# Performance work log

Hardware: AMD Instinct MI355X
Metric: run time of the kernel (lower is better)

The kernel has to match this reference:

```python
import jax, jax.numpy as jnp
import numpy as np
from functools import reduce

N_QUBITS = 12
DIM = 2 ** N_QUBITS          # 4096 state-vector dimension
DEPTH = 6                    # ansatz rotation layers
BATCH = 256
OBSERVE_BITS = (0, 1, 2)     # Pauli-Z expectation on these qubits
INPUT_SCALING = np.pi


def setup_inputs() -> dict:
    key = jax.random.key(0)
    k1, k2 = jax.random.split(key)
    input_tensor = jax.random.uniform(k1, (BATCH, N_QUBITS), dtype=jnp.float32)
    # param_init_range = (-pi/depth, pi/depth)
    thetas = jax.random.normal(k2, (DEPTH, N_QUBITS), dtype=jnp.float32) * (np.pi / DEPTH)
    return {"input_tensor": input_tensor, "thetas": thetas}


def _ry(theta):
    # RY(theta) = [[cos t/2, -sin t/2], [sin t/2, cos t/2]]
    h = theta * 0.5
    c, s = jnp.cos(h), jnp.sin(h)
    return jnp.stack([jnp.stack([c, -s]), jnp.stack([s, c])]).astype(jnp.complex64)


def _cnot_ladder_perm():
    # CNOT(i -> i+1) for i = 0..n-2; each CNOT is a basis permutation that
    # flips the target bit when the control bit is 1. Compose permutations
    # (applied in reverse order so state_out = state_in[perm]). Qubit 0 is the
    # leftmost kron factor, i.e. bit position n-1-q of the basis index.
    perm = np.arange(DIM)
    for cq, tq in reversed([(i, i + 1) for i in range(N_QUBITS - 1)]):
        cbit, tbit = N_QUBITS - 1 - cq, N_QUBITS - 1 - tq
        flip = ((perm >> cbit) & 1) == 1
        perm = np.where(flip, perm ^ (1 << tbit), perm)
    return jnp.asarray(perm)


_PERM = _cnot_ladder_perm()


def _forward(input_tensor, thetas):
    # --- encoder: RY(pi * x_q) applied to |0...0> gives a product state ---
    half = input_tensor * (INPUT_SCALING * 0.5)          # [B, n] half-angles
    c, s = jnp.cos(half), jnp.sin(half)
    psi = jnp.ones((BATCH, 1), dtype=jnp.complex64)
    for q in range(N_QUBITS):                            # fixed small loop over qubits
        amp = jnp.stack([c[:, q], s[:, q]], axis=-1).astype(jnp.complex64)  # [B, 2]
        psi = (psi[:, :, None] * amp[:, None, :]).reshape(BATCH, -1)
    state = psi.T                                        # [DIM, B] complex64

    # --- ansatz: per-depth full-unitary (kron of per-qubit gates) mm, then CNOT ladder ---
    for d in range(DEPTH):
        U = reduce(jnp.kron, [_ry(thetas[d, q]) for q in range(N_QUBITS)])  # [DIM, DIM]
        state = U @ state                                # Hamiltonian @ state (torch.mm)
        state = state[_PERM]                             # entangling CNOT ladder

    # --- observer: <Z_q> on each observed qubit ---
    probs = state.real ** 2 + state.imag ** 2            # [DIM, B]
    idx = jnp.arange(DIM)
    zdiag = jnp.stack([1.0 - 2.0 * ((idx >> (N_QUBITS - 1 - q)) & 1)
                       for q in OBSERVE_BITS]).astype(jnp.float32)          # [K, DIM]
    return jnp.einsum('kn,nb->bk', zdiag, probs)         # [B, K]


def reference(input_tensor, thetas):
    return _forward(input_tensor, thetas)
```

## Files before the change

### kernel.cpp

```cpp
#include <hip/hip_runtime.h>
#include <math.h>
#include <type_traits>

#define NQ     12
#define DIM    4096
#define DEPTH  6
#define NBATCH 256
#define NT     512
#define NREG   8


__host__ __device__ constexpr unsigned axmask(int d, int b) {
    unsigned m = 1u << b;
    for (int i = 0; i < d; ++i) m = (m ^ (m >> 1)) & 0xFFFu;
    return m;
}
__host__ __device__ constexpr unsigned selmask(int d, int b) {
    unsigned m = 1u << b;
    for (int i = 0; i < 16 - d; ++i) m = (m ^ ((m << 1) & 0xFFFu)) & 0xFFFu;
    return m;
}
__host__ __device__ constexpr int cpopc(unsigned v) {
    int c = 0; while (v) { c += (int)(v & 1u); v >>= 1; } return c;
}

template<int I, int N, class F>
__device__ __forceinline__ void sfor(F&& f) {
    if constexpr (I < N) {
        f(std::integral_constant<int, I>{});
        sfor<I + 1, N>(static_cast<F&&>(f));
    }
}

template<int CTRL>
__device__ __forceinline__ float dppx(float v) {
    int iv = __float_as_int(v);
    return __int_as_float(__builtin_amdgcn_update_dpp(iv, iv, CTRL, 0xF, 0xF, false));
}
template<int M4>
__device__ __forceinline__ float lxor_low(float v) {
    static_assert(M4 >= 1 && M4 <= 15, "low mask");
    if constexpr      (M4 == 1)  return dppx<0xB1>(v);
    else if constexpr (M4 == 2)  return dppx<0x4E>(v);
    else if constexpr (M4 == 3)  return dppx<0x1B>(v);
    else if constexpr (M4 == 7)  return dppx<0x141>(v);
    else if constexpr (M4 == 15) return dppx<0x140>(v);
    else if constexpr ((M4 & 8) == 0)
        return lxor_low<M4 ^ 7>(dppx<0x141>(v));
    else
        return lxor_low<M4 ^ 15>(dppx<0x140>(v));
}
template<int MASK>
__device__ __forceinline__ float lxor(float v) {
    static_assert(MASK > 0 && MASK < 64, "lane mask");
    if constexpr (MASK >= 32) {
        return __shfl_xor(v, MASK, 64);
    } else if constexpr (MASK >= 16) {
        return __int_as_float(__builtin_amdgcn_ds_swizzle(__float_as_int(v),
                                                          (MASK << 10) | 0x1F));
    } else {
        return lxor_low<MASK>(v);
    }
}

__device__ __forceinline__ int lad(int t, int k) {
    return t * 8 + 4 * (k ^ ((t >> 2) & 1));
}

template<int D, int B>
__device__ __forceinline__ void gate_reg(float (&st)[NREG], int tid, float t) {
    constexpr unsigned V = axmask(D, B), M = selmask(D, B);
    static_assert((V >> 3) == 0 && V != 0, "reg gate");
    constexpr int VR = (int)V;
    constexpr unsigned MR = M & 7u, MT = M >> 3;
    const float tp = (__popc(MT & (unsigned)tid) & 1) ? t : -t;
    const float tn = -tp;
    sfor<0, NREG>([&](auto RC) {
        constexpr int r = RC.value, r2 = r ^ VR;
        if constexpr (r2 > r) {
            constexpr bool p0 = (cpopc(MR & (unsigned)r)  & 1) != 0;
            constexpr bool p1 = (cpopc(MR & (unsigned)r2) & 1) != 0;
            float a0 = st[r];
            st[r]  = fmaf(p0 ? tn : tp, st[r2], st[r]);
            st[r2] = fmaf(p1 ? tn : tp, a0,     st[r2]);
        }
    });
}

template<int D, int B>
__device__ __forceinline__ void gate_lane(float (&st)[NREG], int tid, float t) {
    constexpr unsigned V = axmask(D, B), M = selmask(D, B);
    constexpr int VT = (int)(V >> 3), VR = (int)(V & 7u);
    static_assert(VT > 0 && VT < 64, "intra-wave gate");
    static_assert((M & 7u) == 0, "no reg bits in selector for b>=3");
    const float tp = (__popc((M >> 3) & (unsigned)tid) & 1) ? t : -t;
    if constexpr (VR == 0) {
        sfor<0, NREG>([&](auto RC) {
            constexpr int r = RC.value;
            float p = lxor<VT>(st[r]);
            st[r] = fmaf(tp, p, st[r]);
        });
    } else {
        sfor<0, NREG>([&](auto RC) {
            constexpr int r = RC.value, r2 = r ^ VR;
            if constexpr (r2 > r) {
                float pa = lxor<VT>(st[r2]);
                float pb = lxor<VT>(st[r]);
                st[r]  = fmaf(tp, pa, st[r]);
                st[r2] = fmaf(tp, pb, st[r2]);
            }
        });
    }
}

template<int D>
__device__ __forceinline__ void gate9x(float (&st)[NREG], int tid, float t,
                                       float* __restrict__ lds9) {
    constexpr unsigned V = axmask(D, 9), M = selmask(D, 9);
    static_assert((V & 7u) == 0 && (M & 7u) == 0, "b9 reg-pure-free");
    constexpr int T = (int)(V >> 3);
    static_assert(T >= 64 && T < 512, "b9 crosses waves");
    const float tp = (__popc((M >> 3) & (unsigned)tid) & 1) ? t : -t;
    float* buf = lds9 + (D & 1) * DIM;
    sfor<0, 2>([&](auto KC) {
        constexpr int k = KC.value;
        *reinterpret_cast<float4*>(&buf[lad(tid, k)]) =
            make_float4(st[4*k], st[4*k+1], st[4*k+2], st[4*k+3]);
    });
    __syncthreads();
    const int p = tid ^ T;
    sfor<0, 2>([&](auto KC) {
        constexpr int k = KC.value;
        float4 pv = *reinterpret_cast<const float4*>(&buf[lad(p, k)]);
        st[4*k+0] = fmaf(tp, pv.x, st[4*k+0]);
        st[4*k+1] = fmaf(tp, pv.y, st[4*k+1]);
        st[4*k+2] = fmaf(tp, pv.z, st[4*k+2]);
        st[4*k+3] = fmaf(tp, pv.w, st[4*k+3]);
    });
}

template<int D>
__device__ __forceinline__ void cross2(float (&st)[NREG], int tid,
                                       float t1, float t2,
                                       float* __restrict__ lds2) {
    constexpr unsigned V1 = axmask(D, 11), V2 = axmask(D, 10);
    constexpr unsigned M1 = selmask(D, 11), M2 = selmask(D, 10);
    static_assert((V1 & 7u) == 0 && (V2 & 7u) == 0, "cross axes reg-free");
    static_assert((M1 & 7u) == 0 && (M2 & 7u) == 0, "cross masks reg-free");
    constexpr int T1 = (int)(V1 >> 3), T2 = (int)(V2 >> 3);
    static_assert((cpopc(M1 & V2) & 1) == 0, "kC sign identity");

    const float t1p = (__popc((M1 >> 3) & (unsigned)tid) & 1) ? t1 : -t1;
    const float t2p = (__popc((M2 >> 3) & (unsigned)tid) & 1) ? t2 : -t2;
    const float t12 = t1p * t2p;

    float* buf = lds2 + (D & 1) * DIM;
    sfor<0, 2>([&](auto KC) {
        constexpr int k = KC.value;
        *reinterpret_cast<float4*>(&buf[lad(tid, k)]) =
            make_float4(st[4*k], st[4*k+1], st[4*k+2], st[4*k+3]);
    });
    __syncthreads();
    const int p1 = tid ^ T1, p2 = tid ^ T2, p3 = tid ^ (T1 ^ T2);
    sfor<0, 2>([&](auto KC) {
        constexpr int k = KC.value;
        float4 A  = *reinterpret_cast<const float4*>(&buf[lad(p1, k)]);
        float4 Bv = *reinterpret_cast<const float4*>(&buf[lad(p2, k)]);
        float4 Cv = *reinterpret_cast<const float4*>(&buf[lad(p3, k)]);
        float t;
        t = fmaf(t1p, A.x, st[4*k+0]); t = fmaf(t2p, Bv.x, t); st[4*k+0] = fmaf(t12, Cv.x, t);
        t = fmaf(t1p, A.y, st[4*k+1]); t = fmaf(t2p, Bv.y, t); st[4*k+1] = fmaf(t12, Cv.y, t);
        t = fmaf(t1p, A.z, st[4*k+2]); t = fmaf(t2p, Bv.z, t); st[4*k+2] = fmaf(t12, Cv.z, t);
        t = fmaf(t1p, A.w, st[4*k+3]); t = fmaf(t2p, Bv.w, t); st[4*k+3] = fmaf(t12, Cv.w, t);
    });
}

template<int D>
__device__ __forceinline__ void depth_apply(float (&st)[NREG], int tid,
                                            const float* __restrict__ tsh,
                                            float* __restrict__ lds2,
                                            float* __restrict__ lds9) {
    float4 ta = *reinterpret_cast<const float4*>(&tsh[D * 12 + 0]);
    float4 tb = *reinterpret_cast<const float4*>(&tsh[D * 12 + 4]);
    float4 tc = *reinterpret_cast<const float4*>(&tsh[D * 12 + 8]);
    float tq[12] = {ta.x, ta.y, ta.z, ta.w, tb.x, tb.y, tb.z, tb.w,
                    tc.x, tc.y, tc.z, tc.w};
    cross2<D>(st, tid, tq[0], tq[1], lds2);
    gate9x<D>(st, tid, tq[2], lds9);
    sfor<3, 12>([&](auto QC) {
        constexpr int Q = QC.value, B = 11 - Q;
        if constexpr (B >= 3) gate_lane<D, B>(st, tid, tq[Q]);
        else                  gate_reg <D, B>(st, tid, tq[Q]);
    });
}

__global__ __launch_bounds__(NT, 2)
void qnet_kernel(const float* __restrict__ x,
                 const float* __restrict__ thetas,
                 float* __restrict__ out)
{
    __shared__ __align__(16) float lds2[2 * DIM];
    __shared__ __align__(16) float lds9[2 * DIM];
    __shared__ __align__(16) float tsh[80];
    __shared__ __align__(16) float csh[80];
    __shared__ float red[8];

    const int b   = blockIdx.x;
    const int tid = threadIdx.x;

    if (tid < 72) {
        float rev = thetas[tid] * 0.07957747154594767f;
        float cc  = __builtin_amdgcn_cosf(rev);
        float ss  = __builtin_amdgcn_sinf(rev);
        csh[tid] = cc;
        tsh[tid] = ss * __builtin_amdgcn_rcpf(cc);
    }

    const float4* xv = reinterpret_cast<const float4*>(x + b * 12);
    float4 xa = xv[0], xb = xv[1], xc = xv[2];
    float xs[12] = {xa.x, xa.y, xa.z, xa.w, xb.x, xb.y, xb.z, xb.w,
                    xc.x, xc.y, xc.z, xc.w};
    float cq[12], sq[12];
    sfor<0, 12>([&](auto QC) {
        constexpr int q = QC.value;
        float rev = xs[q] * 0.25f;
        sq[q] = __builtin_amdgcn_sinf(rev);
        cq[q] = __builtin_amdgcn_cosf(rev);
    });

    float la = 1.0f;
    sfor<0, 9>([&](auto IC) {
        constexpr int i = IC.value;
        la *= ((tid >> i) & 1) ? sq[8 - i] : cq[8 - i];
    });
    float st[NREG];
    st[0] = la;
    sfor<0, 3>([&](auto IC) {
        constexpr int i = IC.value;
        sfor<0, (1 << i)>([&](auto KC) {
            constexpr int k = KC.value;
            float base = st[k];
            st[k + (1 << i)] = base * sq[11 - i];
            st[k]            = base * cq[11 - i];
        });
    });

    __syncthreads();

    sfor<0, 6>([&](auto DC) {
        depth_apply<DC.value>(st, tid, tsh, lds2, lds9);
    });

    float sc = 1.0f;
    sfor<0, 18>([&](auto IC) {
        constexpr int i = IC.value;
        float4 c4 = *reinterpret_cast<const float4*>(&csh[4 * i]);
        sc *= (c4.x * c4.y) * (c4.z * c4.w);
    });

    float tot = 0.0f;
    sfor<0, NREG>([&](auto RC) {
        constexpr int r = RC.value;
        tot = fmaf(st[r], st[r], tot);
    });
    tot *= sc * sc;

    float v = tot;
    v += lxor<1>(v);
    v += lxor<2>(v);
    v += lxor<4>(v);
    v += lxor<8>(v);
    v += lxor<16>(v);
    v += lxor<32>(v);
    const int w = tid >> 6;
    if ((tid & 63) == 0) red[w] = v;
    __syncthreads();
    if (tid < 3) {
        float acc = 0.0f;
        #pragma unroll
        for (int ww = 0; ww < 8; ++ww) {
            int par = (tid == 0) ? ((ww >> 2) & 1)
                    : (tid == 1) ? ((ww >> 1) & 1)
                    :              (((ww >> 2) ^ ww) & 1);
            acc += par ? -red[ww] : red[ww];
        }
        out[b * 3 + tid] = acc;
    }
}

extern "C" void kernel_launch(void* const* d_in, const int* in_sizes, int n_in,
                              void* d_out, int out_size, void* d_ws, size_t ws_size,
                              hipStream_t stream) {
    (void)in_sizes; (void)n_in; (void)out_size; (void)d_ws; (void)ws_size;
    const float* x      = (const float*)d_in[0];
    const float* thetas = (const float*)d_in[1];
    float* out          = (float*)d_out;

    qnet_kernel<<<dim3(NBATCH), dim3(NT), 0, stream>>>(x, thetas, out);
}
```

Before: 14.41 us.

## Fuse three cross-thread qubit gates into one LDS exchange and use permlane swaps

Merges the separate qubit-9 LDS exchange into the existing two-qubit cross-wave step, so each depth applies the three cross-thread gates as a single 8-term combination after one shared-memory store and one barrier. This removes one __syncthreads and one store/read round per depth and halves LDS allocation, which may help occupancy. In exchange each thread now reads seven float4 neighbours instead of three plus one, raising LDS read traffic and FMA count. It also replaces shfl_xor/ds_swizzle lane exchanges with permlane16/32 swap builtins when the compiler provides them, and decomposes masks that span several lane bits.

```diff
diff --git a/kernel.cpp b/kernel.cpp
--- a/kernel.cpp
+++ b/kernel.cpp
@@ -8,6 +8,16 @@
 #define NBATCH 256
 #define NT     512
 #define NREG   8
+
+#if defined(__has_builtin)
+#  if __has_builtin(__builtin_amdgcn_permlane16_swap) && __has_builtin(__builtin_amdgcn_permlane32_swap)
+#    define USE_PERMLANE 1
+#  else
+#    define USE_PERMLANE 0
+#  endif
+#else
+#  define USE_PERMLANE 0
+#endif
 
 
 __host__ __device__ constexpr unsigned axmask(int d, int b) {
@@ -50,6 +60,29 @@
     else
         return lxor_low<M4 ^ 15>(dppx<0x140>(v));
 }
+
+#if USE_PERMLANE
+typedef unsigned u32x2 __attribute__((ext_vector_type(2)));
+__device__ __forceinline__ float plx16(float v) {
+    unsigned u = __float_as_uint(v);
+    u32x2 r = __builtin_amdgcn_permlane16_swap(u, u, false, false);
+    return __uint_as_float(r[0] ^ r[1] ^ u);
+}
+__device__ __forceinline__ float plx32(float v) {
+    unsigned u = __float_as_uint(v);
+    u32x2 r = __builtin_amdgcn_permlane32_swap(u, u, false, false);
+    return __uint_as_float(r[0] ^ r[1] ^ u);
+}
+template<int MASK>
+__device__ __forceinline__ float lxor(float v) {
+    static_assert(MASK > 0 && MASK < 64, "lane mask");
+    float r = v;
+    if constexpr (MASK & 32) r = plx32(r);
+    if constexpr (MASK & 16) r = plx16(r);
+    if constexpr (MASK & 15) r = lxor_low<MASK & 15>(r);
+    return r;
+}
+#else
 template<int MASK>
 __device__ __forceinline__ float lxor(float v) {
     static_assert(MASK > 0 && MASK < 64, "lane mask");
@@ -62,6 +95,7 @@
         return lxor_low<MASK>(v);
     }
 }
+#endif
 
 __device__ __forceinline__ int lad(int t, int k) {
     return t * 8 + 4 * (k ^ ((t >> 2) & 1));
@@ -114,45 +148,27 @@
 }
 
 template<int D>
-__device__ __forceinline__ void gate9x(float (&st)[NREG], int tid, float t,
-                                       float* __restrict__ lds9) {
-    constexpr unsigned V = axmask(D, 9), M = selmask(D, 9);
-    static_assert((V & 7u) == 0 && (M & 7u) == 0, "b9 reg-pure-free");
-    constexpr int T = (int)(V >> 3);
-    static_assert(T >= 64 && T < 512, "b9 crosses waves");
-    const float tp = (__popc((M >> 3) & (unsigned)tid) & 1) ? t : -t;
-    float* buf = lds9 + (D & 1) * DIM;
-    sfor<0, 2>([&](auto KC) {
-        constexpr int k = KC.value;
-        *reinterpret_cast<float4*>(&buf[lad(tid, k)]) =
-            make_float4(st[4*k], st[4*k+1], st[4*k+2], st[4*k+3]);
-    });
-    __syncthreads();
-    const int p = tid ^ T;
-    sfor<0, 2>([&](auto KC) {
-        constexpr int k = KC.value;
-        float4 pv = *reinterpret_cast<const float4*>(&buf[lad(p, k)]);
-        st[4*k+0] = fmaf(tp, pv.x, st[4*k+0]);
-        st[4*k+1] = fmaf(tp, pv.y, st[4*k+1]);
-        st[4*k+2] = fmaf(tp, pv.z, st[4*k+2]);
-        st[4*k+3] = fmaf(tp, pv.w, st[4*k+3]);
-    });
-}
-
-template<int D>
-__device__ __forceinline__ void cross2(float (&st)[NREG], int tid,
-                                       float t1, float t2,
+__device__ __forceinline__ void cross3(float (&st)[NREG], int tid,
+                                       float t1, float t2, float t9,
                                        float* __restrict__ lds2) {
-    constexpr unsigned V1 = axmask(D, 11), V2 = axmask(D, 10);
-    constexpr unsigned M1 = selmask(D, 11), M2 = selmask(D, 10);
-    static_assert((V1 & 7u) == 0 && (V2 & 7u) == 0, "cross axes reg-free");
-    static_assert((M1 & 7u) == 0 && (M2 & 7u) == 0, "cross masks reg-free");
-    constexpr int T1 = (int)(V1 >> 3), T2 = (int)(V2 >> 3);
-    static_assert((cpopc(M1 & V2) & 1) == 0, "kC sign identity");
-
-    const float t1p = (__popc((M1 >> 3) & (unsigned)tid) & 1) ? t1 : -t1;
-    const float t2p = (__popc((M2 >> 3) & (unsigned)tid) & 1) ? t2 : -t2;
-    const float t12 = t1p * t2p;
+    constexpr unsigned V1 = axmask(D, 11), V2 = axmask(D, 10), V9 = axmask(D, 9);
+    constexpr unsigned M1 = selmask(D, 11), M2 = selmask(D, 10), M9 = selmask(D, 9);
+    static_assert(((V1 | V2 | V9) & 7u) == 0, "cross axes reg-free");
+    static_assert(((M1 | M2 | M9) & 7u) == 0, "cross masks reg-free");
+    constexpr int T1 = (int)(V1 >> 3), T2 = (int)(V2 >> 3), T9 = (int)(V9 >> 3);
+    static_assert(T1 > 0 && T2 > 0 && T9 > 0, "thread-crossing");
+    constexpr int p12 = cpopc(M2 & V1) & 1;
+    constexpr int p19 = cpopc(M9 & V1) & 1;
+    constexpr int p29 = cpopc(M9 & V2) & 1;
+    constexpr int p123 = (p12 + cpopc(M9 & (V1 ^ V2))) & 1;
+
+    const float e1 = (__popc((M1 >> 3) & (unsigned)tid) & 1) ? t1 : -t1;
+    const float e2 = (__popc((M2 >> 3) & (unsigned)tid) & 1) ? t2 : -t2;
+    const float e9 = (__popc((M9 >> 3) & (unsigned)tid) & 1) ? t9 : -t9;
+    const float k12  = (p12  ? -1.f : 1.f) * e1 * e2;
+    const float k19  = (p19  ? -1.f : 1.f) * e1 * e9;
+    const float k29  = (p29  ? -1.f : 1.f) * e2 * e9;
+    const float k123 = (p123 ? -1.f : 1.f) * e1 * e2 * e9;
 
     float* buf = lds2 + (D & 1) * DIM;
     sfor<0, 2>([&](auto KC) {
@@ -161,32 +177,49 @@
             make_float4(st[4*k], st[4*k+1], st[4*k+2], st[4*k+3]);
     });
     __syncthreads();
-    const int p1 = tid ^ T1, p2 = tid ^ T2, p3 = tid ^ (T1 ^ T2);
+    const int q1 = tid ^ T1,        q2 = tid ^ T2,        q9 = tid ^ T9;
+    const int q12 = tid ^ (T1^T2),  q19 = tid ^ (T1^T9),  q29 = tid ^ (T2^T9);
+    const int q123 = tid ^ (T1^T2^T9);
     sfor<0, 2>([&](auto KC) {
         constexpr int k = KC.value;
-        float4 A  = *reinterpret_cast<const float4*>(&buf[lad(p1, k)]);
-        float4 Bv = *reinterpret_cast<const float4*>(&buf[lad(p2, k)]);
-        float4 Cv = *reinterpret_cast<const float4*>(&buf[lad(p3, k)]);
-        float t;
-        t = fmaf(t1p, A.x, st[4*k+0]); t = fmaf(t2p, Bv.x, t); st[4*k+0] = fmaf(t12, Cv.x, t);
-        t = fmaf(t1p, A.y, st[4*k+1]); t = fmaf(t2p, Bv.y, t); st[4*k+1] = fmaf(t12, Cv.y, t);
-        t = fmaf(t1p, A.z, st[4*k+2]); t = fmaf(t2p, Bv.z, t); st[4*k+2] = fmaf(t12, Cv.z, t);
-        t = fmaf(t1p, A.w, st[4*k+3]); t = fmaf(t2p, Bv.w, t); st[4*k+3] = fmaf(t12, Cv.w, t);
+        float4 A1 = *reinterpret_cast<const float4*>(&buf[lad(q1,   k)]);
+        float4 A2 = *reinterpret_cast<const float4*>(&buf[lad(q2,   k)]);
+        float4 A9 = *reinterpret_cast<const float4*>(&buf[lad(q9,   k)]);
+        float4 B2 = *reinterpret_cast<const float4*>(&buf[lad(q12,  k)]);
+        float4 B9 = *reinterpret_cast<const float4*>(&buf[lad(q19,  k)]);
+        float4 C9 = *reinterpret_cast<const float4*>(&buf[lad(q29,  k)]);
+        float4 Dv = *reinterpret_cast<const float4*>(&buf[lad(q123, k)]);
+        sfor<0, 4>([&](auto EC) {
+            constexpr int e = EC.value;
+            const float a1 = (e==0)?A1.x:(e==1)?A1.y:(e==2)?A1.z:A1.w;
+            const float a2 = (e==0)?A2.x:(e==1)?A2.y:(e==2)?A2.z:A2.w;
+            const float a9 = (e==0)?A9.x:(e==1)?A9.y:(e==2)?A9.z:A9.w;
+            const float b2 = (e==0)?B2.x:(e==1)?B2.y:(e==2)?B2.z:B2.w;
+            const float b9 = (e==0)?B9.x:(e==1)?B9.y:(e==2)?B9.z:B9.w;
+            const float c9 = (e==0)?C9.x:(e==1)?C9.y:(e==2)?C9.z:C9.w;
+            const float dv = (e==0)?Dv.x:(e==1)?Dv.y:(e==2)?Dv.z:Dv.w;
+            float t = st[4*k+e];
+            t = fmaf(e1,   a1, t);
+            t = fmaf(e2,   a2, t);
+            t = fmaf(e9,   a9, t);
+            t = fmaf(k12,  b2, t);
+            t = fmaf(k19,  b9, t);
+            t = fmaf(k29,  c9, t);
+            st[4*k+e] = fmaf(k123, dv, t);
+        });
     });
 }
 
 template<int D>
 __device__ __forceinline__ void depth_apply(float (&st)[NREG], int tid,
                                             const float* __restrict__ tsh,
-                                            float* __restrict__ lds2,
-                                            float* __restrict__ lds9) {
+                                            float* __restrict__ lds2) {
     float4 ta = *reinterpret_cast<const float4*>(&tsh[D * 12 + 0]);
     float4 tb = *reinterpret_cast<const float4*>(&tsh[D * 12 + 4]);
     float4 tc = *reinterpret_cast<const float4*>(&tsh[D * 12 + 8]);
     float tq[12] = {ta.x, ta.y, ta.z, ta.w, tb.x, tb.y, tb.z, tb.w,
                     tc.x, tc.y, tc.z, tc.w};
-    cross2<D>(st, tid, tq[0], tq[1], lds2);
-    gate9x<D>(st, tid, tq[2], lds9);
+    cross3<D>(st, tid, tq[0], tq[1], tq[2], lds2);
     sfor<3, 12>([&](auto QC) {
         constexpr int Q = QC.value, B = 11 - Q;
         if constexpr (B >= 3) gate_lane<D, B>(st, tid, tq[Q]);
@@ -200,7 +233,6 @@
                  float* __restrict__ out)
 {
     __shared__ __align__(16) float lds2[2 * DIM];
-    __shared__ __align__(16) float lds9[2 * DIM];
     __shared__ __align__(16) float tsh[80];
     __shared__ __align__(16) float csh[80];
     __shared__ float red[8];
@@ -248,7 +280,7 @@
     __syncthreads();
 
     sfor<0, 6>([&](auto DC) {
-        depth_apply<DC.value>(st, tid, tsh, lds2, lds9);
+        depth_apply<DC.value>(st, tid, tsh, lds2);
     });
 
     float sc = 1.0f;
```

New measurement: 16.42 us. 14.0% more time.

## Use 1024 threads with 4 amplitudes each and pair high-qubit gates via LDS

Applied to the files above, without the earlier changes.

Doubles the threads per block to 1024 and halves the per-thread register state from 8 to 4 amplitudes, remapping the qubit-to-thread/register bit layout. The single-qubit cross-wave gate for bit 9 is folded with bit 8 into a second fused two-gate LDS exchange, so each depth still uses two LDS barriers. The aim is more parallelism and shorter per-thread serial gate chains. The cost is larger reductions (16 waves), one block per CU, and more shuffle traffic per amplitude.

```diff
diff --git a/kernel.cpp b/kernel.cpp
--- a/kernel.cpp
+++ b/kernel.cpp
@@ -6,8 +6,8 @@
 #define DIM    4096
 #define DEPTH  6
 #define NBATCH 256
-#define NT     512
-#define NREG   8
+#define NT     1024
+#define NREG   4
 
 
 __host__ __device__ constexpr unsigned axmask(int d, int b) {
@@ -63,16 +63,12 @@
     }
 }
 
-__device__ __forceinline__ int lad(int t, int k) {
-    return t * 8 + 4 * (k ^ ((t >> 2) & 1));
-}
-
 template<int D, int B>
 __device__ __forceinline__ void gate_reg(float (&st)[NREG], int tid, float t) {
     constexpr unsigned V = axmask(D, B), M = selmask(D, B);
-    static_assert((V >> 3) == 0 && V != 0, "reg gate");
+    static_assert((V >> 2) == 0 && V != 0, "reg gate");
     constexpr int VR = (int)V;
-    constexpr unsigned MR = M & 7u, MT = M >> 3;
+    constexpr unsigned MR = M & 3u, MT = M >> 2;
     const float tp = (__popc(MT & (unsigned)tid) & 1) ? t : -t;
     const float tn = -tp;
     sfor<0, NREG>([&](auto RC) {
@@ -90,10 +86,10 @@
 template<int D, int B>
 __device__ __forceinline__ void gate_lane(float (&st)[NREG], int tid, float t) {
     constexpr unsigned V = axmask(D, B), M = selmask(D, B);
-    constexpr int VT = (int)(V >> 3), VR = (int)(V & 7u);
+    constexpr int VT = (int)(V >> 2), VR = (int)(V & 3u);
     static_assert(VT > 0 && VT < 64, "intra-wave gate");
-    static_assert((M & 7u) == 0, "no reg bits in selector for b>=3");
-    const float tp = (__popc((M >> 3) & (unsigned)tid) & 1) ? t : -t;
+    static_assert((M & 3u) == 0, "no reg bits in selector for b>=2");
+    const float tp = (__popc((M >> 2) & (unsigned)tid) & 1) ? t : -t;
     if constexpr (VR == 0) {
         sfor<0, NREG>([&](auto RC) {
             constexpr int r = RC.value;
@@ -113,97 +109,69 @@
     }
 }
 
-template<int D>
-__device__ __forceinline__ void gate9x(float (&st)[NREG], int tid, float t,
-                                       float* __restrict__ lds9) {
-    constexpr unsigned V = axmask(D, 9), M = selmask(D, 9);
-    static_assert((V & 7u) == 0 && (M & 7u) == 0, "b9 reg-pure-free");
-    constexpr int T = (int)(V >> 3);
-    static_assert(T >= 64 && T < 512, "b9 crosses waves");
-    const float tp = (__popc((M >> 3) & (unsigned)tid) & 1) ? t : -t;
-    float* buf = lds9 + (D & 1) * DIM;
-    sfor<0, 2>([&](auto KC) {
-        constexpr int k = KC.value;
-        *reinterpret_cast<float4*>(&buf[lad(tid, k)]) =
-            make_float4(st[4*k], st[4*k+1], st[4*k+2], st[4*k+3]);
-    });
-    __syncthreads();
-    const int p = tid ^ T;
-    sfor<0, 2>([&](auto KC) {
-        constexpr int k = KC.value;
-        float4 pv = *reinterpret_cast<const float4*>(&buf[lad(p, k)]);
-        st[4*k+0] = fmaf(tp, pv.x, st[4*k+0]);
-        st[4*k+1] = fmaf(tp, pv.y, st[4*k+1]);
-        st[4*k+2] = fmaf(tp, pv.z, st[4*k+2]);
-        st[4*k+3] = fmaf(tp, pv.w, st[4*k+3]);
-    });
-}
-
-template<int D>
+template<int D, int BH, int BL>
 __device__ __forceinline__ void cross2(float (&st)[NREG], int tid,
                                        float t1, float t2,
-                                       float* __restrict__ lds2) {
-    constexpr unsigned V1 = axmask(D, 11), V2 = axmask(D, 10);
-    constexpr unsigned M1 = selmask(D, 11), M2 = selmask(D, 10);
-    static_assert((V1 & 7u) == 0 && (V2 & 7u) == 0, "cross axes reg-free");
-    static_assert((M1 & 7u) == 0 && (M2 & 7u) == 0, "cross masks reg-free");
-    constexpr int T1 = (int)(V1 >> 3), T2 = (int)(V2 >> 3);
-    static_assert((cpopc(M1 & V2) & 1) == 0, "kC sign identity");
-
-    const float t1p = (__popc((M1 >> 3) & (unsigned)tid) & 1) ? t1 : -t1;
-    const float t2p = (__popc((M2 >> 3) & (unsigned)tid) & 1) ? t2 : -t2;
-    const float t12 = t1p * t2p;
-
-    float* buf = lds2 + (D & 1) * DIM;
-    sfor<0, 2>([&](auto KC) {
-        constexpr int k = KC.value;
-        *reinterpret_cast<float4*>(&buf[lad(tid, k)]) =
-            make_float4(st[4*k], st[4*k+1], st[4*k+2], st[4*k+3]);
-    });
+                                       float* __restrict__ buf) {
+    constexpr unsigned V1 = axmask(D, BH), V2 = axmask(D, BL);
+    constexpr unsigned M1 = selmask(D, BH), M2 = selmask(D, BL);
+    static_assert((V1 & 3u) == 0 && (V2 & 3u) == 0, "cross axes reg-free");
+    static_assert((M1 & 3u) == 0 && (M2 & 3u) == 0, "cross masks reg-free");
+    constexpr int T1 = (int)(V1 >> 2), T2 = (int)(V2 >> 2);
+    static_assert(T1 > 0 && T2 > 0, "thread-crossing");
+    constexpr int s12 = cpopc(M1 & V2) & 1;
+
+    const float t1p = (__popc((M1 >> 2) & (unsigned)tid) & 1) ? t1 : -t1;
+    const float t2p = (__popc((M2 >> 2) & (unsigned)tid) & 1) ? t2 : -t2;
+    const float t12 = (s12 ? -1.f : 1.f) * t1p * t2p;
+
+    *reinterpret_cast<float4*>(&buf[tid * 4]) =
+        make_float4(st[0], st[1], st[2], st[3]);
     __syncthreads();
-    const int p1 = tid ^ T1, p2 = tid ^ T2, p3 = tid ^ (T1 ^ T2);
-    sfor<0, 2>([&](auto KC) {
-        constexpr int k = KC.value;
-        float4 A  = *reinterpret_cast<const float4*>(&buf[lad(p1, k)]);
-        float4 Bv = *reinterpret_cast<const float4*>(&buf[lad(p2, k)]);
-        float4 Cv = *reinterpret_cast<const float4*>(&buf[lad(p3, k)]);
-        float t;
-        t = fmaf(t1p, A.x, st[4*k+0]); t = fmaf(t2p, Bv.x, t); st[4*k+0] = fmaf(t12, Cv.x, t);
-        t = fmaf(t1p, A.y, st[4*k+1]); t = fmaf(t2p, Bv.y, t); st[4*k+1] = fmaf(t12, Cv.y, t);
-        t = fmaf(t1p, A.z, st[4*k+2]); t = fmaf(t2p, Bv.z, t); st[4*k+2] = fmaf(t12, Cv.z, t);
-        t = fmaf(t1p, A.w, st[4*k+3]); t = fmaf(t2p, Bv.w, t); st[4*k+3] = fmaf(t12, Cv.w, t);
-    });
+    const int p1 = (tid ^ T1) * 4, p2 = (tid ^ T2) * 4,
+              p3 = (tid ^ (T1 ^ T2)) * 4;
+    float4 A  = *reinterpret_cast<const float4*>(&buf[p1]);
+    float4 Bv = *reinterpret_cast<const float4*>(&buf[p2]);
+    float4 Cv = *reinterpret_cast<const float4*>(&buf[p3]);
+    float t;
+    t = fmaf(t1p, A.x, st[0]); t = fmaf(t2p, Bv.x, t); st[0] = fmaf(t12, Cv.x, t);
+    t = fmaf(t1p, A.y, st[1]); t = fmaf(t2p, Bv.y, t); st[1] = fmaf(t12, Cv.y, t);
+    t = fmaf(t1p, A.z, st[2]); t = fmaf(t2p, Bv.z, t); st[2] = fmaf(t12, Cv.z, t);
+    t = fmaf(t1p, A.w, st[3]); t = fmaf(t2p, Bv.w, t); st[3] = fmaf(t12, Cv.w, t);
 }
 
 template<int D>
 __device__ __forceinline__ void depth_apply(float (&st)[NREG], int tid,
                                             const float* __restrict__ tsh,
-                                            float* __restrict__ lds2,
-                                            float* __restrict__ lds9) {
+                                            float* __restrict__ ldsA,
+                                            float* __restrict__ ldsB) {
     float4 ta = *reinterpret_cast<const float4*>(&tsh[D * 12 + 0]);
     float4 tb = *reinterpret_cast<const float4*>(&tsh[D * 12 + 4]);
     float4 tc = *reinterpret_cast<const float4*>(&tsh[D * 12 + 8]);
     float tq[12] = {ta.x, ta.y, ta.z, ta.w, tb.x, tb.y, tb.z, tb.w,
                     tc.x, tc.y, tc.z, tc.w};
-    cross2<D>(st, tid, tq[0], tq[1], lds2);
-    gate9x<D>(st, tid, tq[2], lds9);
-    sfor<3, 12>([&](auto QC) {
-        constexpr int Q = QC.value, B = 11 - Q;
-        if constexpr (B >= 3) gate_lane<D, B>(st, tid, tq[Q]);
-        else                  gate_reg <D, B>(st, tid, tq[Q]);
-    });
-}
-
-__global__ __launch_bounds__(NT, 2)
+    cross2<D, 11, 10>(st, tid, tq[0], tq[1], ldsA + (D & 1) * DIM);
+    cross2<D,  9,  8>(st, tid, tq[2], tq[3], ldsB + (D & 1) * DIM);
+    gate_lane<D, 7>(st, tid, tq[4]);
+    gate_lane<D, 6>(st, tid, tq[5]);
+    gate_lane<D, 5>(st, tid, tq[6]);
+    gate_lane<D, 4>(st, tid, tq[7]);
+    gate_lane<D, 3>(st, tid, tq[8]);
+    gate_lane<D, 2>(st, tid, tq[9]);
+    gate_reg<D, 1>(st, tid, tq[10]);
+    gate_reg<D, 0>(st, tid, tq[11]);
+}
+
+__global__ __launch_bounds__(NT, 1)
 void qnet_kernel(const float* __restrict__ x,
                  const float* __restrict__ thetas,
                  float* __restrict__ out)
 {
-    __shared__ __align__(16) float lds2[2 * DIM];
-    __shared__ __align__(16) float lds9[2 * DIM];
+    __shared__ __align__(16) float ldsA[2 * DIM];
+    __shared__ __align__(16) float ldsB[2 * DIM];
     __shared__ __align__(16) float tsh[80];
     __shared__ __align__(16) float csh[80];
-    __shared__ float red[8];
+    __shared__ float red[16];
 
     const int b   = blockIdx.x;
     const int tid = threadIdx.x;
@@ -229,13 +197,13 @@
     });
 
     float la = 1.0f;
-    sfor<0, 9>([&](auto IC) {
+    sfor<0, 10>([&](auto IC) {
         constexpr int i = IC.value;
-        la *= ((tid >> i) & 1) ? sq[8 - i] : cq[8 - i];
+        la *= ((tid >> i) & 1) ? sq[9 - i] : cq[9 - i];
     });
     float st[NREG];
     st[0] = la;
-    sfor<0, 3>([&](auto IC) {
+    sfor<0, 2>([&](auto IC) {
         constexpr int i = IC.value;
         sfor<0, (1 << i)>([&](auto KC) {
             constexpr int k = KC.value;
@@ -248,7 +216,7 @@
     __syncthreads();
 
     sfor<0, 6>([&](auto DC) {
-        depth_apply<DC.value>(st, tid, tsh, lds2, lds9);
+        depth_apply<DC.value>(st, tid, tsh, ldsA, ldsB);
     });
 
     float sc = 1.0f;
@@ -278,10 +246,10 @@
     if (tid < 3) {
         float acc = 0.0f;
         #pragma unroll
-        for (int ww = 0; ww < 8; ++ww) {
-            int par = (tid == 0) ? ((ww >> 2) & 1)
-                    : (tid == 1) ? ((ww >> 1) & 1)
-                    :              (((ww >> 2) ^ ww) & 1);
+        for (int ww = 0; ww < 16; ++ww) {
+            int par = (tid == 0) ? ((ww >> 3) & 1)
+                    : (tid == 1) ? ((ww >> 2) & 1)
+                    :              (((ww >> 3) ^ (ww >> 1)) & 1);
             acc += par ? -red[ww] : red[ww];
         }
         out[b * 3 + tid] = acc;
```

Result: slower. 14.96 us (+3.9%).
